# Kernel tuning notes

Measured on AMD Instinct MI355X. Metric: run time of the kernel, lower is better.

## Reference

```python
import jax, jax.numpy as jnp
import numpy as np

NEG_BIG = -9e15

def setup_inputs() -> dict:
    key = jax.random.key(0)
    k1, k2, k3, k4 = jax.random.split(key, 4)
    B, N, C, D = 8, 2048, 128, 128
    x = jax.random.normal(k1, (B, N, C), dtype=jnp.float32)
    adj = jax.random.randint(k2, (N, N), 0, 2, dtype=jnp.int32)
    W = jax.random.normal(k3, (D, C), dtype=jnp.float32) * (1.0 / np.sqrt(C))
    a = jax.random.normal(k4, (1, 2 * D), dtype=jnp.float32) * (1.0 / np.sqrt(2 * D))
    return {"x": x, "adj": adj, "W": W, "a": a}

def reference(x, adj, W, a):
    # Wh: [B,N,D]
    Wh = jnp.einsum('bnc,dc->bnd', x, W)
    D = Wh.shape[-1]
    a1, a2 = a[0, :D], a[0, D:]
    # e[b,i,j] = leakyrelu(a1.Wh_i + a2.Wh_j)  (algebraic split of cat([Wh_i,Wh_j]) @ a)
    f1 = Wh @ a1  # [B,N]
    f2 = Wh @ a2  # [B,N]
    e = jax.nn.leaky_relu(f1[:, :, None] + f2[:, None, :], negative_slope=0.2)  # [B,N,N]
    e = jnp.where(adj[None] > 0, e, NEG_BIG)
    attention = jax.nn.softmax(e, axis=-1)
    h_prime = jnp.einsum('bij,bjd->bid', attention, Wh)
    return jax.nn.elu(h_prime)
```

## Files before the change

kernel.cpp:

```cpp
#include <hip/hip_runtime.h>
#include <hip/hip_bf16.h>
#include <math.h>

#define BB 8
#define NN 2048
#define CC 128
#define DD 128

typedef __attribute__((ext_vector_type(8))) short short8;
typedef __attribute__((ext_vector_type(4))) float f32x4;

static __device__ __forceinline__ unsigned short f2bf(float f) {
    __hip_bfloat16 h = __float2bfloat16(f);
    return *reinterpret_cast<unsigned short*>(&h);
}
static __device__ __forceinline__ float bf2f(unsigned short u) {
    __hip_bfloat16 h = *reinterpret_cast<__hip_bfloat16*>(&u);
    return __bfloat162float(h);
}

#define PACKB 256
__global__ __launch_bounds__(256) void prep_wh_kernel(
    const int* __restrict__ adj, unsigned int* __restrict__ padj,
    const float* __restrict__ x, const float* __restrict__ W,
    const float* __restrict__ a,
    unsigned short* __restrict__ WhbT,
    float* __restrict__ f1, float* __restrict__ E2g, float* __restrict__ G2g)
{
    __shared__ unsigned short Whs[128 * 136];
    __shared__ unsigned short Wls[128 * 136];
    const int bx  = blockIdx.x;
    const int tid = threadIdx.x;

    if (bx < PACKB) {
        const int wid = bx * 256 + tid;
        #pragma unroll
        for (int rep = 0; rep < 2; ++rep) {
            const int word = wid + rep * 65536;
            const int4* src = (const int4*)adj + (size_t)word * 8;
            unsigned int m = 0;
            #pragma unroll
            for (int k = 0; k < 8; ++k) {
                int4 v = src[k];
                m |= (v.x > 0 ? 1u : 0u) << (k * 4);
                m |= (v.y > 0 ? 1u : 0u) << (k * 4 + 1);
                m |= (v.z > 0 ? 1u : 0u) << (k * 4 + 2);
                m |= (v.w > 0 ? 1u : 0u) << (k * 4 + 3);
            }
            padj[word] = m;
        }
        return;
    }

    const int g  = bx - PACKB;
    const int b  = g & 7;
    const int n0 = (g >> 3) * 64;

    #pragma unroll
    for (int k = 0; k < 16; ++k) {
        const int e   = tid + 256 * k;
        float4 wv = *(const float4*)&W[e * 4];
        const int row = e >> 5;
        const int col = (e & 31) * 4;
        ushort4 hv, lv;
        hv.x = f2bf(wv.x); lv.x = f2bf(wv.x - bf2f(hv.x));
        hv.y = f2bf(wv.y); lv.y = f2bf(wv.y - bf2f(hv.y));
        hv.z = f2bf(wv.z); lv.z = f2bf(wv.z - bf2f(hv.z));
        hv.w = f2bf(wv.w); lv.w = f2bf(wv.w - bf2f(hv.w));
        *(ushort4*)&Whs[row * 136 + col] = hv;
        *(ushort4*)&Wls[row * 136 + col] = lv;
    }
    __syncthreads();

    const int w    = tid >> 6;
    const int lane = tid & 63;
    const int fr   = lane & 15, fk = lane >> 4;
    const int n    = n0 + w * 16 + fr;

    short8 bh[4], bl[4];
    const float* xrow = &x[((size_t)(b * NN) + n) * CC];
    #pragma unroll
    for (int ks = 0; ks < 4; ++ks) {
        float xv[8];
        *(float4*)&xv[0] = *(const float4*)&xrow[(ks * 4 + fk) * 8];
        *(float4*)&xv[4] = *(const float4*)&xrow[(ks * 4 + fk) * 8 + 4];
        #pragma unroll
        for (int e = 0; e < 8; ++e) {
            unsigned short h = f2bf(xv[e]);
            bh[ks][e] = (short)h;
            bl[ks][e] = (short)f2bf(xv[e] - bf2f(h));
        }
    }

    f32x4 acc[8];
    #pragma unroll
    for (int dt = 0; dt < 8; ++dt) acc[dt] = (f32x4){0.f, 0.f, 0.f, 0.f};

    #pragma unroll
    for (int dt = 0; dt < 8; ++dt) {
        #pragma unroll
        for (int ks = 0; ks < 4; ++ks) {
            const int off = (dt * 16 + fr) * 136 + (ks * 4 + fk) * 8;
            short8 aH = *(const short8*)&Whs[off];
            short8 aL = *(const short8*)&Wls[off];
            acc[dt] = __builtin_amdgcn_mfma_f32_16x16x32_bf16(aH, bh[ks], acc[dt], 0, 0, 0);
            acc[dt] = __builtin_amdgcn_mfma_f32_16x16x32_bf16(aH, bl[ks], acc[dt], 0, 0, 0);
            acc[dt] = __builtin_amdgcn_mfma_f32_16x16x32_bf16(aL, bh[ks], acc[dt], 0, 0, 0);
        }
    }

    float p1 = 0.f, p2 = 0.f;
    #pragma unroll
    for (int dt = 0; dt < 8; ++dt) {
        #pragma unroll
        for (int r = 0; r < 4; ++r) {
            const int d = dt * 16 + fk * 4 + r;
            p1 += acc[dt][r] * a[d];
            p2 += acc[dt][r] * a[DD + d];
        }
    }
    p1 += __shfl_xor(p1, 16); p1 += __shfl_xor(p1, 32);
    p2 += __shfl_xor(p2, 16); p2 += __shfl_xor(p2, 32);
    if (fk == 0) {
        f1[b * NN + n]  = p1;
        E2g[b * NN + n] = __expf(p2);
        G2g[b * NN + n] = __expf(0.2f * p2);
    }

    #pragma unroll
    for (int dt = 0; dt < 8; ++dt) {
        #pragma unroll
        for (int r = 0; r < 4; ++r) {
            const int d = dt * 16 + fk * 4 + r;
            WhbT[((size_t)(b * 128 + d)) * NN + n] = f2bf(acc[dt][r]);
        }
    }
}

__global__ __launch_bounds__(256) void gat_kernel(
    const unsigned short* __restrict__ WhbT,
    const unsigned int* __restrict__ padj,
    const float* __restrict__ f1,
    const float* __restrict__ E2g, const float* __restrict__ G2g,
    float* __restrict__ out)
{
    constexpr int NC = NN / 64;
    __shared__ __align__(16) unsigned char smem[57600];
    unsigned short* Bs0 = (unsigned short*)smem;
    unsigned short* Bs1 = (unsigned short*)(smem + 16384);
    unsigned short* Ps0 = (unsigned short*)(smem + 32768);
    unsigned short* Ps1 = (unsigned short*)(smem + 36864);
    float* E2s  = (float*)(smem + 40960);
    float* G2s  = (float*)(smem + 49152);
    float* Srow = (float*)(smem + 57344);
    float* Sred = (float*)(smem + 57472);
    float* T    = (float*)smem;

    const int tid  = threadIdx.x;
    const int gblk = blockIdx.x;
    const int b    = gblk & 7;
    const int i0   = (gblk >> 3) * 32;

    #pragma unroll
    for (int k = 0; k < NN / 256; ++k) {
        E2s[tid + 256 * k] = E2g[b * NN + tid + 256 * k];
        G2s[tid + 256 * k] = G2g[b * NN + tid + 256 * k];
    }

    const int prow = tid >> 3;
    const int pjb  = tid & 7;
    const float f1r = f1[b * NN + i0 + prow];
    const float E1r = __expf(f1r);
    const float G1r = __expf(0.2f * f1r);
    const int psw = ((pjb ^ (prow & 7)) << 3);
    const unsigned int* padjRow = padj + (size_t)(i0 + prow) * 64;

    const int w    = tid >> 6;
    const int lane = tid & 63;
    const int fr   = lane & 15;
    const int fk   = lane >> 4;
    f32x4 acc00 = {0.f,0.f,0.f,0.f}, acc01 = {0.f,0.f,0.f,0.f};
    f32x4 acc10 = {0.f,0.f,0.f,0.f}, acc11 = {0.f,0.f,0.f,0.f};
    float s_part = 0.f;

    const size_t wbase = (size_t)b * 128 * NN;
    const int g0 = tid,       gd0 = g0 >> 3, gj0 = (g0 & 7) * 8;
    const int g1 = tid + 256, gd1 = g1 >> 3, gj1 = (g1 & 7) * 8;
    const int g2 = tid + 512, gd2 = g2 >> 3, gj2 = (g2 & 7) * 8;
    const int g3 = tid + 768, gd3 = g3 >> 3, gj3 = (g3 & 7) * 8;
    const int sw0 = gd0 * 64 + ((((g0) & 7) ^ (gd0 & 7)) << 3);
    const int sw1 = gd1 * 64 + ((((g1) & 7) ^ (gd1 & 7)) << 3);
    const int sw2 = gd2 * 64 + ((((g2) & 7) ^ (gd2 & 7)) << 3);
    const int sw3 = gd3 * 64 + ((((g3) & 7) ^ (gd3 & 7)) << 3);

    uint4 brA0, brA1, brA2, brA3, brB0, brB1, brB2, brB3;
    unsigned int pwA, pwB;

#define LOADSET(s, c) do {                                                   \
        br##s##0 = *(const uint4*)&WhbT[wbase + (size_t)gd0 * NN + (c) * 64 + gj0]; \
        br##s##1 = *(const uint4*)&WhbT[wbase + (size_t)gd1 * NN + (c) * 64 + gj1]; \
        br##s##2 = *(const uint4*)&WhbT[wbase + (size_t)gd2 * NN + (c) * 64 + gj2]; \
        br##s##3 = *(const uint4*)&WhbT[wbase + (size_t)gd3 * NN + (c) * 64 + gj3]; \
        pw##s    = padjRow[(c) * 2 + (pjb >> 2)];                            \
    } while (0)

#define PSTAGE(Bsb, Psb, s, c) do {                                          \
        float4 eA = *(const float4*)&E2s[(c) * 64 + pjb * 8];                \
        float4 eB = *(const float4*)&E2s[(c) * 64 + pjb * 8 + 4];            \
        float4 gA = *(const float4*)&G2s[(c) * 64 + pjb * 8];                \
        float4 gB = *(const float4*)&G2s[(c) * 64 + pjb * 8 + 4];            \
        float ev[8], gv[8];                                                  \
        *(float4*)&ev[0] = eA; *(float4*)&ev[4] = eB;                        \
        *(float4*)&gv[0] = gA; *(float4*)&gv[4] = gB;                        \
        unsigned int pbits = (pw##s >> ((pjb & 3) << 3)) & 0xffu;            \
        unsigned short pks[8];                                               \
        float ssum = 0.f;                                                    \
        _Pragma("unroll")                                                    \
        for (int e = 0; e < 8; ++e) {                                        \
            float mv = E1r * ev[e];                                          \
            float gg = G1r * gv[e];                                          \
            float wv = fmaxf(mv, gg);                                        \
            wv = ((pbits >> e) & 1u) ? wv : 0.f;                             \
            unsigned short bw = f2bf(wv);                                    \
            pks[e] = bw;                                                     \
            ssum += bf2f(bw);                                                \
        }                                                                    \
        s_part += ssum;                                                      \
        *(uint4*)&Bsb[sw0] = br##s##0;                                       \
        *(uint4*)&Bsb[sw1] = br##s##1;                                       \
        *(uint4*)&Bsb[sw2] = br##s##2;                                       \
        *(uint4*)&Bsb[sw3] = br##s##3;                                       \
        uint4 pv;                                                            \
        pv.x = (unsigned int)pks[0] | ((unsigned int)pks[1] << 16);          \
        pv.y = (unsigned int)pks[2] | ((unsigned int)pks[3] << 16);          \
        pv.z = (unsigned int)pks[4] | ((unsigned int)pks[5] << 16);          \
        pv.w = (unsigned int)pks[6] | ((unsigned int)pks[7] << 16);          \
        *(uint4*)&Psb[prow * 64 + psw] = pv;                                 \
    } while (0)

#define MFMAC(Bsb, Psb) do {                                                 \
        __builtin_amdgcn_s_setprio(1);                                       \
        _Pragma("unroll")                                                    \
        for (int ks = 0; ks < 2; ++ks) {                                     \
            const int jbl = ks * 4 + fk;                                     \
            const int sb  = ((jbl ^ (fr & 7)) << 3);                         \
            short8 aF0 = *(const short8*)&Psb[fr * 64 + sb];                 \
            short8 aF1 = *(const short8*)&Psb[(16 + fr) * 64 + sb];          \
            short8 bF0 = *(const short8*)&Bsb[(w * 32 + fr) * 64 + sb];      \
            short8 bF1 = *(const short8*)&Bsb[(w * 32 + 16 + fr) * 64 + sb]; \
            acc00 = __builtin_amdgcn_mfma_f32_16x16x32_bf16(aF0, bF0, acc00, 0, 0, 0); \
            acc01 = __builtin_amdgcn_mfma_f32_16x16x32_bf16(aF0, bF1, acc01, 0, 0, 0); \
            acc10 = __builtin_amdgcn_mfma_f32_16x16x32_bf16(aF1, bF0, acc10, 0, 0, 0); \
            acc11 = __builtin_amdgcn_mfma_f32_16x16x32_bf16(aF1, bF1, acc11, 0, 0, 0); \
        }                                                                    \
        __builtin_amdgcn_s_setprio(0);                                       \
    } while (0)

    LOADSET(A, 0);
    __syncthreads();
    PSTAGE(Bs0, Ps0, A, 0);
    LOADSET(B, 1);
    __syncthreads();

    #pragma unroll 1
    for (int cc = 0; cc < NC; cc += 2) {
        PSTAGE(Bs1, Ps1, B, cc + 1);
        if (cc + 2 < NC) LOADSET(A, cc + 2);
        MFMAC(Bs0, Ps0);
        __syncthreads();
        if (cc + 2 < NC) PSTAGE(Bs0, Ps0, A, cc + 2);
        if (cc + 3 < NC) LOADSET(B, cc + 3);
        MFMAC(Bs1, Ps1);
        __syncthreads();
    }

#undef LOADSET
#undef PSTAGE
#undef MFMAC

    {
        float v = s_part;
        v += __shfl_xor(v, 1); v += __shfl_xor(v, 2); v += __shfl_xor(v, 4);
        if (pjb == 0) Srow[prow] = v;
    }
    __syncthreads();
    if (tid < 32) Sred[tid] = 1.0f / Srow[tid];
    __syncthreads();

    #pragma unroll
    for (int it = 0; it < 2; ++it) {
        #pragma unroll
        for (int dt = 0; dt < 2; ++dt) {
            f32x4 av = (it == 0) ? (dt == 0 ? acc00 : acc01)
                                 : (dt == 0 ? acc10 : acc11);
            #pragma unroll
            for (int r = 0; r < 4; ++r) {
                const int i = it * 16 + fk * 4 + r;
                const int d = w * 32 + dt * 16 + fr;
                float hv = av[r] * Sred[i];
                hv = (hv > 0.f) ? hv : expm1f(hv);
                T[i * 132 + d] = hv;
            }
        }
    }
    __syncthreads();

    #pragma unroll
    for (int k = 0; k < 4; ++k) {
        const int g   = tid + 256 * k;
        const int row = g >> 5;
        const int d4  = (g & 31) * 4;
        float4 h = *(const float4*)&T[row * 132 + d4];
        *(float4*)&out[((size_t)(b * NN) + i0 + row) * DD + d4] = h;
    }
}

extern "C" void kernel_launch(void* const* d_in, const int* in_sizes, int n_in,
                              void* d_out, int out_size, void* d_ws, size_t ws_size,
                              hipStream_t stream) {
    const float* x   = (const float*)d_in[0];
    const int*   adj = (const int*)d_in[1];
    const float* W   = (const float*)d_in[2];
    const float* a   = (const float*)d_in[3];
    float* out = (float*)d_out;

    char* p = (char*)d_ws;
    unsigned short* WhbT = (unsigned short*)p; p += (size_t)BB * NN * DD * 2;
    float* f1  = (float*)p; p += (size_t)BB * NN * 4;
    float* E2g = (float*)p; p += (size_t)BB * NN * 4;
    float* G2g = (float*)p; p += (size_t)BB * NN * 4;
    unsigned int* padj = (unsigned int*)p;    p += (size_t)NN * 64 * 4;

    prep_wh_kernel<<<PACKB + (NN / 64) * BB, 256, 0, stream>>>(
        adj, padj, x, W, a, WhbT, f1, E2g, G2g);
    gat_kernel<<<(NN / 32) * BB, 256, 0, stream>>>(
        WhbT, padj, f1, E2g, G2g, out);
}
```

Before: 37.68 us.

## Load Wh B-fragments directly from global into registers, bypassing LDS staging

Each wave now reads its MFMA B operand (transposed bf16 Wh) straight from global memory into registers instead of staging the whole 128x64 tile through shared memory. This removes the LDS writes and reads for B and cuts shared memory from about 57KB to about 25KB, which may allow more blocks per CU. The adjacency loads are split from the B loads, and B for a chunk is now issued only after that chunk's MFMAs, so less time is available to hide its latency. Global reads become 16-byte per-lane row accesses with less coalescing, and the lack of reuse across the 4 waves may raise L2 traffic.

```diff
diff --git a/kernel.cpp b/kernel.cpp
--- a/kernel.cpp
+++ b/kernel.cpp
@@ -145,15 +145,13 @@
     float* __restrict__ out)
 {
     constexpr int NC = NN / 64;
-    __shared__ __align__(16) unsigned char smem[57600];
-    unsigned short* Bs0 = (unsigned short*)smem;
-    unsigned short* Bs1 = (unsigned short*)(smem + 16384);
-    unsigned short* Ps0 = (unsigned short*)(smem + 32768);
-    unsigned short* Ps1 = (unsigned short*)(smem + 36864);
-    float* E2s  = (float*)(smem + 40960);
-    float* G2s  = (float*)(smem + 49152);
-    float* Srow = (float*)(smem + 57344);
-    float* Sred = (float*)(smem + 57472);
+    __shared__ __align__(16) unsigned char smem[24832];
+    unsigned short* Ps0 = (unsigned short*)smem;
+    unsigned short* Ps1 = (unsigned short*)(smem + 4096);
+    float* E2s  = (float*)(smem + 8192);
+    float* G2s  = (float*)(smem + 16384);
+    float* Srow = (float*)(smem + 24576);
+    float* Sred = (float*)(smem + 24704);
     float* T    = (float*)smem;
 
     const int tid  = threadIdx.x;
@@ -183,28 +181,21 @@
     f32x4 acc10 = {0.f,0.f,0.f,0.f}, acc11 = {0.f,0.f,0.f,0.f};
     float s_part = 0.f;
 
-    const size_t wbase = (size_t)b * 128 * NN;
-    const int g0 = tid,       gd0 = g0 >> 3, gj0 = (g0 & 7) * 8;
-    const int g1 = tid + 256, gd1 = g1 >> 3, gj1 = (g1 & 7) * 8;
-    const int g2 = tid + 512, gd2 = g2 >> 3, gj2 = (g2 & 7) * 8;
-    const int g3 = tid + 768, gd3 = g3 >> 3, gj3 = (g3 & 7) * 8;
-    const int sw0 = gd0 * 64 + ((((g0) & 7) ^ (gd0 & 7)) << 3);
-    const int sw1 = gd1 * 64 + ((((g1) & 7) ^ (gd1 & 7)) << 3);
-    const int sw2 = gd2 * 64 + ((((g2) & 7) ^ (gd2 & 7)) << 3);
-    const int sw3 = gd3 * 64 + ((((g3) & 7) ^ (gd3 & 7)) << 3);
-
-    uint4 brA0, brA1, brA2, brA3, brB0, brB1, brB2, brB3;
+    const unsigned short* wrow0 =
+        WhbT + (size_t)b * 128 * NN + (size_t)(w * 32 + fr) * NN + fk * 8;
+    const unsigned short* wrow1 = wrow0 + (size_t)16 * NN;
+
+    short8 bA00, bA01, bA10, bA11, bB00, bB01, bB10, bB11;
     unsigned int pwA, pwB;
 
-#define LOADSET(s, c) do {                                                   \
-        br##s##0 = *(const uint4*)&WhbT[wbase + (size_t)gd0 * NN + (c) * 64 + gj0]; \
-        br##s##1 = *(const uint4*)&WhbT[wbase + (size_t)gd1 * NN + (c) * 64 + gj1]; \
-        br##s##2 = *(const uint4*)&WhbT[wbase + (size_t)gd2 * NN + (c) * 64 + gj2]; \
-        br##s##3 = *(const uint4*)&WhbT[wbase + (size_t)gd3 * NN + (c) * 64 + gj3]; \
-        pw##s    = padjRow[(c) * 2 + (pjb >> 2)];                            \
+#define BLOAD(s, c) do {                                                     \
+        b##s##00 = *(const short8*)(wrow0 + (c) * 64);                       \
+        b##s##01 = *(const short8*)(wrow1 + (c) * 64);                       \
+        b##s##10 = *(const short8*)(wrow0 + (c) * 64 + 32);                  \
+        b##s##11 = *(const short8*)(wrow1 + (c) * 64 + 32);                  \
     } while (0)
 
-#define PSTAGE(Bsb, Psb, s, c) do {                                          \
+#define PSTAGE(Psb, s, c) do {                                               \
         float4 eA = *(const float4*)&E2s[(c) * 64 + pjb * 8];                \
         float4 eB = *(const float4*)&E2s[(c) * 64 + pjb * 8 + 4];            \
         float4 gA = *(const float4*)&G2s[(c) * 64 + pjb * 8];                \
@@ -226,10 +217,6 @@
             ssum += bf2f(bw);                                                \
         }                                                                    \
         s_part += ssum;                                                      \
-        *(uint4*)&Bsb[sw0] = br##s##0;                                       \
-        *(uint4*)&Bsb[sw1] = br##s##1;                                       \
-        *(uint4*)&Bsb[sw2] = br##s##2;                                       \
-        *(uint4*)&Bsb[sw3] = br##s##3;                                       \
         uint4 pv;                                                            \
         pv.x = (unsigned int)pks[0] | ((unsigned int)pks[1] << 16);          \
         pv.y = (unsigned int)pks[2] | ((unsigned int)pks[3] << 16);          \
@@ -238,43 +225,52 @@
         *(uint4*)&Psb[prow * 64 + psw] = pv;                                 \
     } while (0)
 
-#define MFMAC(Bsb, Psb) do {                                                 \
+#define MFMAC(Psb, s) do {                                                   \
         __builtin_amdgcn_s_setprio(1);                                       \
-        _Pragma("unroll")                                                    \
-        for (int ks = 0; ks < 2; ++ks) {                                     \
-            const int jbl = ks * 4 + fk;                                     \
-            const int sb  = ((jbl ^ (fr & 7)) << 3);                         \
-            short8 aF0 = *(const short8*)&Psb[fr * 64 + sb];                 \
-            short8 aF1 = *(const short8*)&Psb[(16 + fr) * 64 + sb];          \
-            short8 bF0 = *(const short8*)&Bsb[(w * 32 + fr) * 64 + sb];      \
-            short8 bF1 = *(const short8*)&Bsb[(w * 32 + 16 + fr) * 64 + sb]; \
-            acc00 = __builtin_amdgcn_mfma_f32_16x16x32_bf16(aF0, bF0, acc00, 0, 0, 0); \
-            acc01 = __builtin_amdgcn_mfma_f32_16x16x32_bf16(aF0, bF1, acc01, 0, 0, 0); \
-            acc10 = __builtin_amdgcn_mfma_f32_16x16x32_bf16(aF1, bF0, acc10, 0, 0, 0); \
-            acc11 = __builtin_amdgcn_mfma_f32_16x16x32_bf16(aF1, bF1, acc11, 0, 0, 0); \
+        {                                                                    \
+            const int sb0 = (((0 * 4 + fk) ^ (fr & 7)) << 3);                \
+            short8 aF0 = *(const short8*)&Psb[fr * 64 + sb0];                \
+            short8 aF1 = *(const short8*)&Psb[(16 + fr) * 64 + sb0];         \
+            acc00 = __builtin_amdgcn_mfma_f32_16x16x32_bf16(aF0, b##s##00, acc00, 0, 0, 0); \
+            acc01 = __builtin_amdgcn_mfma_f32_16x16x32_bf16(aF0, b##s##01, acc01, 0, 0, 0); \
+            acc10 = __builtin_amdgcn_mfma_f32_16x16x32_bf16(aF1, b##s##00, acc10, 0, 0, 0); \
+            acc11 = __builtin_amdgcn_mfma_f32_16x16x32_bf16(aF1, b##s##01, acc11, 0, 0, 0); \
+        }                                                                    \
+        {                                                                    \
+            const int sb1 = (((1 * 4 + fk) ^ (fr & 7)) << 3);                \
+            short8 aF0 = *(const short8*)&Psb[fr * 64 + sb1];                \
+            short8 aF1 = *(const short8*)&Psb[(16 + fr) * 64 + sb1];         \
+            acc00 = __builtin_amdgcn_mfma_f32_16x16x32_bf16(aF0, b##s##10, acc00, 0, 0, 0); \
+            acc01 = __builtin_amdgcn_mfma_f32_16x16x32_bf16(aF0, b##s##11, acc01, 0, 0, 0); \
+            acc10 = __builtin_amdgcn_mfma_f32_16x16x32_bf16(aF1, b##s##10, acc10, 0, 0, 0); \
+            acc11 = __builtin_amdgcn_mfma_f32_16x16x32_bf16(aF1, b##s##11, acc11, 0, 0, 0); \
         }                                                                    \
         __builtin_amdgcn_s_setprio(0);                                       \
     } while (0)
 
-    LOADSET(A, 0);
-    __syncthreads();
-    PSTAGE(Bs0, Ps0, A, 0);
-    LOADSET(B, 1);
+    pwA = padjRow[(pjb >> 2)];
+    BLOAD(A, 0);
+    __syncthreads();
+    PSTAGE(Ps0, A, 0);
+    pwB = padjRow[2 + (pjb >> 2)];
+    BLOAD(B, 1);
     __syncthreads();
 
     #pragma unroll 1
     for (int cc = 0; cc < NC; cc += 2) {
-        PSTAGE(Bs1, Ps1, B, cc + 1);
-        if (cc + 2 < NC) LOADSET(A, cc + 2);
-        MFMAC(Bs0, Ps0);
+        PSTAGE(Ps1, B, cc + 1);
+        if (cc + 2 < NC) pwA = padjRow[(cc + 2) * 2 + (pjb >> 2)];
+        MFMAC(Ps0, A);
+        if (cc + 2 < NC) BLOAD(A, cc + 2);
         __syncthreads();
-        if (cc + 2 < NC) PSTAGE(Bs0, Ps0, A, cc + 2);
-        if (cc + 3 < NC) LOADSET(B, cc + 3);
-        MFMAC(Bs1, Ps1);
+        if (cc + 2 < NC) PSTAGE(Ps0, A, cc + 2);
+        if (cc + 3 < NC) pwB = padjRow[(cc + 3) * 2 + (pjb >> 2)];
+        MFMAC(Ps1, B);
+        if (cc + 3 < NC) BLOAD(B, cc + 3);
         __syncthreads();
     }
 
-#undef LOADSET
+#undef BLOAD
 #undef PSTAGE
 #undef MFMAC
 
```

Result: slower. 48.32 us (+28.2%).

## Pre-swizzle Wh tiles in global memory and stream them directly into LDS

Applied to the files above, without the earlier changes.

The prep kernel now writes the bf16 Wh values in a chunked, pre-swizzled layout that matches the attention kernel's LDS tile layout. The attention kernel can then use global_load_lds to copy 16-byte pieces straight from global memory into shared memory, with no register staging and no per-thread swizzled LDS stores. This frees registers and VALU work in the main loop. In exchange, the prep kernel's stores become scattered 2-byte writes, and the direct-to-LDS loads are issued right after a barrier, which may shorten the window for hiding their latency.

```diff
diff --git a/kernel.cpp b/kernel.cpp
--- a/kernel.cpp
+++ b/kernel.cpp
@@ -17,6 +17,11 @@
 static __device__ __forceinline__ float bf2f(unsigned short u) {
     __hip_bfloat16 h = *reinterpret_cast<__hip_bfloat16*>(&u);
     return __bfloat162float(h);
+}
+static __device__ __forceinline__ void gload_lds16(const void* g, void* l) {
+    __builtin_amdgcn_global_load_lds(
+        (const __attribute__((address_space(1))) unsigned int*)g,
+        (__attribute__((address_space(3))) unsigned int*)l, 16, 0, 0);
 }
 
 #define PACKB 256
@@ -24,7 +29,7 @@
     const int* __restrict__ adj, unsigned int* __restrict__ padj,
     const float* __restrict__ x, const float* __restrict__ W,
     const float* __restrict__ a,
-    unsigned short* __restrict__ WhbT,
+    unsigned short* __restrict__ WhbTs,
     float* __restrict__ f1, float* __restrict__ E2g, float* __restrict__ G2g)
 {
     __shared__ unsigned short Whs[128 * 136];
@@ -127,18 +132,24 @@
         G2g[b * NN + n] = __expf(0.2f * p2);
     }
 
-    #pragma unroll
-    for (int dt = 0; dt < 8; ++dt) {
-        #pragma unroll
-        for (int r = 0; r < 4; ++r) {
-            const int d = dt * 16 + fk * 4 + r;
-            WhbT[((size_t)(b * 128 + d)) * NN + n] = f2bf(acc[dt][r]);
+    {
+        const int c  = n >> 6;
+        const int jb = (n >> 3) & 7;
+        const int e  = n & 7;
+        unsigned short* dst = WhbTs + ((size_t)(b * 32 + c) << 13) + e;
+        #pragma unroll
+        for (int dt = 0; dt < 8; ++dt) {
+            #pragma unroll
+            for (int r = 0; r < 4; ++r) {
+                const int d = dt * 16 + fk * 4 + r;
+                dst[d * 64 + ((jb ^ (d & 7)) << 3)] = f2bf(acc[dt][r]);
+            }
         }
     }
 }
 
 __global__ __launch_bounds__(256) void gat_kernel(
-    const unsigned short* __restrict__ WhbT,
+    const unsigned short* __restrict__ WhbTs,
     const unsigned int* __restrict__ padj,
     const float* __restrict__ f1,
     const float* __restrict__ E2g, const float* __restrict__ G2g,
@@ -183,28 +194,19 @@
     f32x4 acc10 = {0.f,0.f,0.f,0.f}, acc11 = {0.f,0.f,0.f,0.f};
     float s_part = 0.f;
 
-    const size_t wbase = (size_t)b * 128 * NN;
-    const int g0 = tid,       gd0 = g0 >> 3, gj0 = (g0 & 7) * 8;
-    const int g1 = tid + 256, gd1 = g1 >> 3, gj1 = (g1 & 7) * 8;
-    const int g2 = tid + 512, gd2 = g2 >> 3, gj2 = (g2 & 7) * 8;
-    const int g3 = tid + 768, gd3 = g3 >> 3, gj3 = (g3 & 7) * 8;
-    const int sw0 = gd0 * 64 + ((((g0) & 7) ^ (gd0 & 7)) << 3);
-    const int sw1 = gd1 * 64 + ((((g1) & 7) ^ (gd1 & 7)) << 3);
-    const int sw2 = gd2 * 64 + ((((g2) & 7) ^ (gd2 & 7)) << 3);
-    const int sw3 = gd3 * 64 + ((((g3) & 7) ^ (gd3 & 7)) << 3);
-
-    uint4 brA0, brA1, brA2, brA3, brB0, brB1, brB2, brB3;
+    const char* gch = (const char*)(WhbTs + ((size_t)(b * 32) << 13)) + (w << 12) + lane * 16;
     unsigned int pwA, pwB;
 
-#define LOADSET(s, c) do {                                                   \
-        br##s##0 = *(const uint4*)&WhbT[wbase + (size_t)gd0 * NN + (c) * 64 + gj0]; \
-        br##s##1 = *(const uint4*)&WhbT[wbase + (size_t)gd1 * NN + (c) * 64 + gj1]; \
-        br##s##2 = *(const uint4*)&WhbT[wbase + (size_t)gd2 * NN + (c) * 64 + gj2]; \
-        br##s##3 = *(const uint4*)&WhbT[wbase + (size_t)gd3 * NN + (c) * 64 + gj3]; \
-        pw##s    = padjRow[(c) * 2 + (pjb >> 2)];                            \
+#define BSTAGE(BsDst, c) do {                                                \
+        const char* gsrc = gch + ((size_t)(c) << 14);                        \
+        char* ldst = (char*)(BsDst) + (w << 12);                             \
+        gload_lds16(gsrc,        ldst);                                      \
+        gload_lds16(gsrc + 1024, ldst + 1024);                               \
+        gload_lds16(gsrc + 2048, ldst + 2048);                               \
+        gload_lds16(gsrc + 3072, ldst + 3072);                               \
     } while (0)
 
-#define PSTAGE(Bsb, Psb, s, c) do {                                          \
+#define PSTAGE(Psb, s, c) do {                                               \
         float4 eA = *(const float4*)&E2s[(c) * 64 + pjb * 8];                \
         float4 eB = *(const float4*)&E2s[(c) * 64 + pjb * 8 + 4];            \
         float4 gA = *(const float4*)&G2s[(c) * 64 + pjb * 8];                \
@@ -226,10 +228,6 @@
             ssum += bf2f(bw);                                                \
         }                                                                    \
         s_part += ssum;                                                      \
-        *(uint4*)&Bsb[sw0] = br##s##0;                                       \
-        *(uint4*)&Bsb[sw1] = br##s##1;                                       \
-        *(uint4*)&Bsb[sw2] = br##s##2;                                       \
-        *(uint4*)&Bsb[sw3] = br##s##3;                                       \
         uint4 pv;                                                            \
         pv.x = (unsigned int)pks[0] | ((unsigned int)pks[1] << 16);          \
         pv.y = (unsigned int)pks[2] | ((unsigned int)pks[3] << 16);          \
@@ -256,25 +254,29 @@
         __builtin_amdgcn_s_setprio(0);                                       \
     } while (0)
 
-    LOADSET(A, 0);
-    __syncthreads();
-    PSTAGE(Bs0, Ps0, A, 0);
-    LOADSET(B, 1);
+    BSTAGE(Bs0, 0);
+    pwA = padjRow[(pjb >> 2)];
+    __syncthreads();
+    BSTAGE(Bs1, 1);
+    PSTAGE(Ps0, A, 0);
+    pwB = padjRow[2 + (pjb >> 2)];
     __syncthreads();
 
     #pragma unroll 1
     for (int cc = 0; cc < NC; cc += 2) {
-        PSTAGE(Bs1, Ps1, B, cc + 1);
-        if (cc + 2 < NC) LOADSET(A, cc + 2);
+        PSTAGE(Ps1, B, cc + 1);
+        if (cc + 2 < NC) pwA = padjRow[(cc + 2) * 2 + (pjb >> 2)];
         MFMAC(Bs0, Ps0);
         __syncthreads();
-        if (cc + 2 < NC) PSTAGE(Bs0, Ps0, A, cc + 2);
-        if (cc + 3 < NC) LOADSET(B, cc + 3);
+        if (cc + 2 < NC) BSTAGE(Bs0, cc + 2);
+        if (cc + 2 < NC) PSTAGE(Ps0, A, cc + 2);
+        if (cc + 3 < NC) pwB = padjRow[(cc + 3) * 2 + (pjb >> 2)];
         MFMAC(Bs1, Ps1);
         __syncthreads();
-    }
-
-#undef LOADSET
+        if (cc + 3 < NC) BSTAGE(Bs1, cc + 3);
+    }
+
+#undef BSTAGE
 #undef PSTAGE
 #undef MFMAC
 
@@ -325,14 +327,14 @@
     float* out = (float*)d_out;
 
     char* p = (char*)d_ws;
-    unsigned short* WhbT = (unsigned short*)p; p += (size_t)BB * NN * DD * 2;
+    unsigned short* WhbTs = (unsigned short*)p; p += (size_t)BB * NN * DD * 2;
     float* f1  = (float*)p; p += (size_t)BB * NN * 4;
     float* E2g = (float*)p; p += (size_t)BB * NN * 4;
     float* G2g = (float*)p; p += (size_t)BB * NN * 4;
-    unsigned int* padj = (unsigned int*)p;    p += (size_t)NN * 64 * 4;
+    unsigned int* padj = (unsigned int*)p;     p += (size_t)NN * 64 * 4;
 
     prep_wh_kernel<<<PACKB + (NN / 64) * BB, 256, 0, stream>>>(
-        adj, padj, x, W, a, WhbT, f1, E2g, G2g);
+        adj, padj, x, W, a, WhbTs, f1, E2g, G2g);
     gat_kernel<<<(NN / 32) * BB, 256, 0, stream>>>(
-        WhbT, padj, f1, E2g, G2g, out);
-}
+        WhbTs, padj, f1, E2g, G2g, out);
+}
```

Result: slower. 39.70 us (+5.3%).
